# Performance work log

Measured on AMD Instinct MI355X. Metric: run time of the kernel, lower is better.

Reference implementation:

```python
import math
import jax, jax.numpy as jnp
import numpy as np

B, SEQ, N_EMBD, N_HEAD, MAX_LEN = 2, 2048, 1024, 16, 2048
D_HEAD = N_EMBD // N_HEAD


def setup_inputs() -> dict:
    key = jax.random.key(0)
    k0, k1, k2, k3, k4 = jax.random.split(key, 5)
    x = jax.random.normal(k0, (B, SEQ, N_EMBD), jnp.float32)
    # nn.Linear weights stored [out_features, in_features]; scale ~ kaiming-ish
    s = 1.0 / math.sqrt(N_EMBD)
    Wq = jax.random.normal(k1, (N_EMBD, N_EMBD), jnp.float32) * s
    Wk = jax.random.normal(k2, (N_EMBD, N_EMBD), jnp.float32) * s
    Wv = jax.random.normal(k3, (N_EMBD, N_EMBD), jnp.float32) * s
    Er = jax.random.normal(k4, (MAX_LEN, D_HEAD), jnp.float32)
    return {"x": x, "Wq": Wq, "Wk": Wk, "Wv": Wv, "Er": Er}


def _skew(QEr):
    # QEr: [B, H, S, S]; mask with anti-diagonal tril-flip, then pad/reshape skew
    S = QEr.shape[-1]
    anti = jnp.flip(jnp.tril(jnp.ones((S, S), QEr.dtype)), axis=1)
    QEr = QEr * anti  # masked_fill(mask==0, 0)
    padded = jnp.pad(QEr, ((0, 0), (0, 0), (0, 0), (1, 0)))  # [B,H,S,S+1]
    Bq, H, S_, Sp1 = padded.shape
    return padded.reshape(Bq, H, Sp1, S_)[:, :, 1:, :]  # [B,H,S,S]


def reference(x, Wq, Wk, Wv, Er):
    Bx, S, E = x.shape
    H, d = N_HEAD, D_HEAD

    def proj(W):
        return jnp.einsum('bse,fe->bsf', x, W).reshape(Bx, S, H, d).transpose(0, 2, 1, 3)

    q, k, v = proj(Wq), proj(Wk), proj(Wv)  # [B,H,S,d]
    qk = jnp.einsum('bhqd,bhkd->bhqk', q, k)
    Er_s = Er[MAX_LEN - S:, :]  # [S, d]
    QEr = jnp.einsum('bhqd,rd->bhqr', q, Er_s)  # [B,H,S,S]
    Srel = _skew(QEr)
    attn = (qk + Srel) / math.sqrt(d)
    causal = jnp.tril(jnp.ones((S, S), bool))
    attn = jnp.where(causal, attn, -jnp.inf)
    p = jax.nn.softmax(attn, axis=-1)
    out = jnp.einsum('bhqk,bhkd->bhqd', p, v)
    return out.transpose(0, 2, 1, 3).reshape(Bx, S, E)
```

## Files before the change

### kernel.cpp

```cpp
#include <hip/hip_runtime.h>
#include <hip/hip_bf16.h>
#include <stdint.h>

#define S_LEN 2048
#define EMB   1024
#define NH    16
#define DH    64
#define BATCH 2

typedef short bf16x8 __attribute__((ext_vector_type(8)));
typedef short bf16x4 __attribute__((ext_vector_type(4)));
typedef float f32x4  __attribute__((ext_vector_type(4)));

__device__ __forceinline__ unsigned short f2bf(float f) {
    union { float f; unsigned int u; } v; v.f = f;
    unsigned int r = v.u + 0x7FFFu + ((v.u >> 16) & 1u);
    return (unsigned short)(r >> 16);
}

__device__ __forceinline__ short f2bf_fast(float f) {
    __hip_bfloat16 h = __float2bfloat16(f);
    return *reinterpret_cast<short*>(&h);
}

__device__ __forceinline__ float bf2f(short s) {
    union { unsigned int u; float f; } v;
    v.u = ((unsigned int)(unsigned short)s) << 16;
    return v.f;
}

__device__ __forceinline__ bf16x8 load8f_to_bf(const float* __restrict__ p) {
    const float4* p4 = (const float4*)p;
    float4 x0 = p4[0];
    float4 x1 = p4[1];
    bf16x8 r;
    r[0] = (short)f2bf(x0.x); r[1] = (short)f2bf(x0.y);
    r[2] = (short)f2bf(x0.z); r[3] = (short)f2bf(x0.w);
    r[4] = (short)f2bf(x1.x); r[5] = (short)f2bf(x1.y);
    r[6] = (short)f2bf(x1.z); r[7] = (short)f2bf(x1.w);
    return r;
}

__device__ __forceinline__ void bar_lds() {
    asm volatile("s_waitcnt lgkmcnt(0)" ::: "memory");
    __builtin_amdgcn_sched_barrier(0);
    __builtin_amdgcn_s_barrier();
    __builtin_amdgcn_sched_barrier(0);
}

__device__ __forceinline__ void gload_lds16(const unsigned short* g, unsigned short* l) {
    __builtin_amdgcn_global_load_lds(
        (const __attribute__((address_space(1))) unsigned int*)g,
        (__attribute__((address_space(3))) unsigned int*)l, 16, 0, 0);
}

__global__ __launch_bounds__(256) void cvt_bf16(
    const float* __restrict__ x,  const float* __restrict__ wq,
    const float* __restrict__ wk, const float* __restrict__ wv,
    const float* __restrict__ er,
    unsigned short* __restrict__ xb, unsigned short* __restrict__ wb,
    unsigned short* __restrict__ erb)
{
    const int NX = 4194304 / 8, NW = 1048576 / 8, NE = 131072 / 8;
    const int total = NX + 3 * NW + NE;
    for (int i8 = blockIdx.x * 256 + threadIdx.x; i8 < total; i8 += gridDim.x * 256) {
        const float* src; unsigned short* dst; int off;
        if      (i8 < NX)          { src = x;  dst = xb;            off = i8; }
        else if (i8 < NX + NW)     { src = wq; dst = wb;            off = i8 - NX; }
        else if (i8 < NX + 2 * NW) { src = wk; dst = wb + 1048576;  off = i8 - NX - NW; }
        else if (i8 < NX + 3 * NW) { src = wv; dst = wb + 2097152;  off = i8 - NX - 2 * NW; }
        else                       { src = er; dst = erb;           off = i8 - NX - 3 * NW; }
        ((bf16x8*)dst)[off] = load8f_to_bf(src + (size_t)off * 8);
    }
}

__global__ __launch_bounds__(256) void proj_kernel_bf(
    const unsigned short* __restrict__ xb, const unsigned short* __restrict__ wb,
    unsigned short* __restrict__ Qb, unsigned short* __restrict__ Kb,
    unsigned short* __restrict__ Vt)
{
    __shared__ __align__(16) unsigned short Al[128 * 64];
    __shared__ __align__(16) unsigned short Bl[128 * 64];

    const int tid  = threadIdx.x;
    const int lane = tid & 63;
    const int w    = tid >> 6;
    const int wr   = w >> 1;
    const int wc   = w & 1;
    const int m0   = blockIdx.x * 128;
    const int c0   = blockIdx.y * 128;
    const int wsel = c0 >> 10;
    const int f0   = c0 & 1023;
    const unsigned short* __restrict__ W = wb + (size_t)wsel * 1048576;

    const int lr = lane & 15;
    const int g  = lane >> 4;

    const int srow8 = tid >> 3;
    const int scol  = (((tid & 7) ^ (srow8 & 7))) * 8;

    f32x4 acc[4][4];
#pragma unroll
    for (int i = 0; i < 4; i++)
#pragma unroll
        for (int n = 0; n < 4; n++) acc[i][n] = (f32x4){0.f, 0.f, 0.f, 0.f};

    for (int k0 = 0; k0 < 1024; k0 += 64) {
        __syncthreads();
#pragma unroll
        for (int i = 0; i < 4; i++) {
            gload_lds16(&xb[(size_t)(m0 + i * 32 + srow8) * 1024 + k0 + scol],
                        &Al[(i * 4 + w) * 512]);
            gload_lds16(&W [(size_t)(f0 + i * 32 + srow8) * 1024 + k0 + scol],
                        &Bl[(i * 4 + w) * 512]);
        }
        __syncthreads();

#pragma unroll
        for (int kk = 0; kk < 2; kk++) {
            bf16x8 a[4], b[4];
#pragma unroll
            for (int i = 0; i < 4; i++) {
                int ar = wr * 64 + i * 16 + lr;
                a[i] = *(const bf16x8*)&Al[ar * 64 + (((kk * 4 + g) ^ (ar & 7)) * 8)];
            }
#pragma unroll
            for (int n = 0; n < 4; n++) {
                int br = wc * 64 + n * 16 + lr;
                b[n] = *(const bf16x8*)&Bl[br * 64 + (((kk * 4 + g) ^ (br & 7)) * 8)];
            }
#pragma unroll
            for (int i = 0; i < 4; i++)
#pragma unroll
                for (int n = 0; n < 4; n++)
                    acc[i][n] = __builtin_amdgcn_mfma_f32_16x16x32_bf16(a[i], b[n], acc[i][n], 0, 0, 0);
        }
    }

#pragma unroll
    for (int i = 0; i < 4; i++) {
#pragma unroll
        for (int n = 0; n < 4; n++) {
#pragma unroll
            for (int j = 0; j < 4; j++) {
                int row_m = m0 + wr * 64 + i * 16 + g * 4 + j;
                int c     = c0 + wc * 64 + n * 16 + lr;
                int f     = c & 1023;
                int h     = f >> 6;
                int dd    = f & 63;
                int bb    = row_m >> 11;
                int s     = row_m & 2047;
                int bh    = bb * 16 + h;
                unsigned short bv = f2bf(acc[i][n][j]);
                if (wsel == 0)      Qb[((size_t)bh * 2048 + s) * 64 + dd] = bv;
                else if (wsel == 1) Kb[((size_t)bh * 2048 + s) * 64 + dd] = bv;
                else                Vt[((size_t)bh * 64 + dd) * 2048 + s] = bv;
            }
        }
    }
}

__global__ __launch_bounds__(256) void proj_kernel_f32(
    const float* __restrict__ x,
    const float* __restrict__ Wq, const float* __restrict__ Wk,
    const float* __restrict__ Wv,
    unsigned short* __restrict__ Qb, unsigned short* __restrict__ Kb,
    unsigned short* __restrict__ Vt)
{
    const int tid  = threadIdx.x;
    const int lane = tid & 63;
    const int w    = tid >> 6;
    const int wr   = w >> 1;
    const int wc   = w & 1;
    const int m0   = blockIdx.x * 128 + wr * 64;
    const int c0   = blockIdx.y * 128 + wc * 64;
    const int wsel = c0 >> 10;
    const int f0   = c0 & 1023;
    const float* __restrict__ W = (wsel == 0) ? Wq : (wsel == 1) ? Wk : Wv;

    const int lr = lane & 15;
    const int lk = (lane >> 4) * 8;

    f32x4 acc[4][4];
#pragma unroll
    for (int i = 0; i < 4; i++)
#pragma unroll
        for (int n = 0; n < 4; n++) acc[i][n] = (f32x4){0.f, 0.f, 0.f, 0.f};

    for (int k0 = 0; k0 < 1024; k0 += 32) {
        bf16x8 a[4], b[4];
#pragma unroll
        for (int i = 0; i < 4; i++)
            a[i] = load8f_to_bf(&x[(size_t)(m0 + i * 16 + lr) * 1024 + k0 + lk]);
#pragma unroll
        for (int n = 0; n < 4; n++)
            b[n] = load8f_to_bf(&W[(size_t)(f0 + n * 16 + lr) * 1024 + k0 + lk]);
#pragma unroll
        for (int i = 0; i < 4; i++)
#pragma unroll
            for (int n = 0; n < 4; n++)
                acc[i][n] = __builtin_amdgcn_mfma_f32_16x16x32_bf16(a[i], b[n], acc[i][n], 0, 0, 0);
    }

    const int g = lane >> 4;
#pragma unroll
    for (int i = 0; i < 4; i++) {
#pragma unroll
        for (int n = 0; n < 4; n++) {
#pragma unroll
            for (int j = 0; j < 4; j++) {
                int row_m = m0 + i * 16 + g * 4 + j;
                int c     = c0 + n * 16 + lr;
                int f     = c & 1023;
                int h     = f >> 6;
                int dd    = f & 63;
                int bb    = row_m >> 11;
                int s     = row_m & 2047;
                int bh    = bb * 16 + h;
                unsigned short bv = f2bf(acc[i][n][j]);
                if (wsel == 0)      Qb[((size_t)bh * 2048 + s) * 64 + dd] = bv;
                else if (wsel == 1) Kb[((size_t)bh * 2048 + s) * 64 + dd] = bv;
                else                Vt[((size_t)bh * 64 + dd) * 2048 + s] = bv;
            }
        }
    }
}

__global__ void cvt_er(const float* __restrict__ Er, unsigned short* __restrict__ Erb, int n)
{
    int i = blockIdx.x * 256 + threadIdx.x;
    if (i < n) Erb[i] = f2bf(Er[i]);
}

__global__ __launch_bounds__(256) void attn_kernel(
    const unsigned short* __restrict__ Qb, const unsigned short* __restrict__ Kb,
    const unsigned short* __restrict__ Vt, const unsigned short* __restrict__ Erb,
    float* __restrict__ out)
{
    __shared__ __align__(16) unsigned short Kl[64 * 64];
    __shared__ __align__(16) unsigned short Vl[64 * 64];
    __shared__ __align__(16) unsigned short El[128 * 64];
    __shared__ __align__(16) float          Rt[4][16][80];

    const int tid  = threadIdx.x;
    const int lane = tid & 63;
    const int w    = tid >> 6;

    const int i0  = blockIdx.x;
    const int xcd = i0 & 7;
    const int b2  = (i0 >> 3) & 3;
    const int qt  = 31 - (i0 >> 5);
    const int bh  = (xcd << 2) | b2;

    const int lr = lane & 15;
    const int g  = lane >> 4;
    const int lk = g * 8;

    const unsigned short* __restrict__ Qrow = Qb + (size_t)bh * 2048 * 64;
    const unsigned short* __restrict__ Krow = Kb + (size_t)bh * 2048 * 64;
    const unsigned short* __restrict__ Vrow = Vt + (size_t)bh * 64 * 2048;

    const float SCL = 0.125f * 1.44269504089f;
    const int bb  = bh >> 4;
    const int h   = bh & 15;
    const int q0  = qt * 64;
    const int q0w = q0 + w * 16;
    const int eoff = 48 - 16 * w;
    const int rbT0 = 1984 - q0;

    bf16x8 aq[2];
#pragma unroll
    for (int kk = 0; kk < 2; kk++) {
        bf16x8 q = *(const bf16x8*)&Qrow[(size_t)(q0w + lr) * 64 + kk * 32 + lk];
#pragma unroll
        for (int e = 0; e < 8; e++)
            q[e] = f2bf_fast(bf2f(q[e]) * SCL);
        aq[kk] = q;
    }

    f32x4 o[4];
#pragma unroll
    for (int m = 0; m < 4; m++) o[m] = (f32x4){0.f, 0.f, 0.f, 0.f};
    float mrow = -1e30f, lsum = 0.f;

    bf16x8 sk[2], sv[2], se[4];
    const int o8u = (tid & 7) * 8;

    auto kv_load = [&](int kt) {
        const int k0 = kt * 64;
#pragma unroll
        for (int i = 0; i < 2; i++) {
            int kr = ((i * 256 + tid) >> 3);
            sk[i] = *(const bf16x8*)&Krow[(size_t)(k0 + kr) * 64 + o8u];
        }
#pragma unroll
        for (int i = 0; i < 2; i++) {
            int d = ((i * 256 + tid) >> 3);
            sv[i] = *(const bf16x8*)&Vrow[(size_t)d * 2048 + k0 + o8u];
        }
    };
    auto kv_write = [&]() {
#pragma unroll
        for (int i = 0; i < 2; i++) {
            int kr = ((i * 256 + tid) >> 3);
            *(bf16x8*)&Kl[(kr * 64 + o8u) ^ ((kr & 7) << 3)] = sk[i];
        }
#pragma unroll
        for (int i = 0; i < 2; i++) {
            int d = ((i * 256 + tid) >> 3);
            *(bf16x8*)&Vl[(d * 64 + o8u) ^ ((d & 7) << 3)] = sv[i];
        }
    };
    auto e_load4 = [&](int base) {
#pragma unroll
        for (int i = 0; i < 4; i++) {
            int r = base + ((i * 256 + tid) >> 3);
            int rr = r > 2047 ? 2047 : r;
            se[i] = *(const bf16x8*)&Erb[(size_t)rr * 64 + o8u];
        }
    };
    auto e_load2 = [&](int base) {
#pragma unroll
        for (int i = 0; i < 2; i++) {
            int r = base + ((i * 256 + tid) >> 3);
            int rr = r > 2047 ? 2047 : r;
            se[i] = *(const bf16x8*)&Erb[(size_t)rr * 64 + o8u];
        }
    };
    auto e_write4 = [&](int base) {
#pragma unroll
        for (int i = 0; i < 4; i++) {
            int r = base + ((i * 256 + tid) >> 3);
            int slot = r & 127;
            *(bf16x8*)&El[(slot * 64 + o8u) ^ ((slot & 7) << 3)] = se[i];
        }
    };
    auto e_write2 = [&](int base) {
#pragma unroll
        for (int i = 0; i < 2; i++) {
            int r = base + ((i * 256 + tid) >> 3);
            int slot = r & 127;
            *(bf16x8*)&El[(slot * 64 + o8u) ^ ((slot & 7) << 3)] = se[i];
        }
    };

    kv_load(0);
    e_load4(rbT0);

#pragma unroll 1
    for (int kt = 0; kt <= qt; ++kt) {
        const int ep = ((qt ^ kt ^ 1) & 1) << 6;

        bar_lds();
        kv_write();
        if (kt == 0) e_write4(rbT0);
        else         e_write2(rbT0 + 64 * kt + 64);
        if (kt < qt) {
            kv_load(kt + 1);
            e_load2(rbT0 + 64 * kt + 128);
        }
        bar_lds();

        f32x4 s[4], r[5];
#pragma unroll
        for (int n = 0; n < 4; n++) s[n] = (f32x4){0.f, 0.f, 0.f, 0.f};
#pragma unroll
        for (int n = 0; n < 5; n++) r[n] = (f32x4){0.f, 0.f, 0.f, 0.f};
        __builtin_amdgcn_s_setprio(1);
#pragma unroll
        for (int kk = 0; kk < 2; kk++) {
            bf16x8 kb[4], be[5];
#pragma unroll
            for (int n = 0; n < 4; n++) {
                int kr = n * 16 + lr;
                kb[n] = *(const bf16x8*)&Kl[(kr * 64 + kk * 32 + lk) ^ ((kr & 7) << 3)];
            }
#pragma unroll
            for (int n = 0; n < 5; n++) {
                int er = (eoff + n * 16 + lr + ep) & 127;
                be[n] = *(const bf16x8*)&El[(er * 64 + kk * 32 + lk) ^ ((er & 7) << 3)];
            }
#pragma unroll
            for (int n = 0; n < 4; n++)
                s[n] = __builtin_amdgcn_mfma_f32_16x16x32_bf16(kb[n], aq[kk], s[n], 0, 0, 0);
#pragma unroll
            for (int n = 0; n < 5; n++)
                r[n] = __builtin_amdgcn_mfma_f32_16x16x32_bf16(be[n], aq[kk], r[n], 0, 0, 0);
        }
        __builtin_amdgcn_s_setprio(0);

#pragma unroll
        for (int n = 0; n < 5; n++)
            *(f32x4*)&Rt[w][lr][n * 16 + g * 4] = r[n];

        bar_lds();

        float pmax = -1e30f;
        if (kt != qt) {
#pragma unroll
            for (int n = 0; n < 4; n++)
#pragma unroll
                for (int j = 0; j < 4; j++) {
                    int kl = n * 16 + g * 4 + j;
                    float sc = s[n][j] + Rt[w][lr][kl + 15 - lr];
                    s[n][j] = sc;
                    pmax = fmaxf(pmax, sc);
                }
        } else {
#pragma unroll
            for (int n = 0; n < 4; n++)
#pragma unroll
                for (int j = 0; j < 4; j++) {
                    int kl = n * 16 + g * 4 + j;
                    float sc = s[n][j] + Rt[w][lr][kl + 15 - lr];
                    if (kl > w * 16 + lr) sc = -1e30f;
                    s[n][j] = sc;
                    pmax = fmaxf(pmax, sc);
                }
        }

        if (__any(pmax > mrow + 4.0f)) {
            pmax = fmaxf(pmax, __shfl_xor(pmax, 16));
            pmax = fmaxf(pmax, __shfl_xor(pmax, 32));
            float mn   = fmaxf(mrow, pmax);
            float corr = exp2f(mrow - mn);
            mrow = mn;
            lsum *= corr;
#pragma unroll
            for (int j = 0; j < 4; j++) {
                float cj = __shfl(corr, g * 4 + j);
#pragma unroll
                for (int m = 0; m < 4; m++) o[m][j] *= cj;
            }
        }

        float rs = 0.f;
        bf16x4 pa[4];
#pragma unroll
        for (int n = 0; n < 4; n++)
#pragma unroll
            for (int j = 0; j < 4; j++) {
                float pv = exp2f(s[n][j] - mrow);
                rs += pv;
                pa[n][j] = f2bf_fast(pv);
            }
        lsum += rs;

        __builtin_amdgcn_s_setprio(1);
#pragma unroll
        for (int m = 0; m < 4; m++) {
#pragma unroll
            for (int n = 0; n < 4; n++) {
                int d = 16 * m + lr;
                bf16x4 vb = *(const bf16x4*)&Vl[(d * 64 + 16 * n + 4 * g) ^ ((d & 7) << 3)];
                o[m] = __builtin_amdgcn_mfma_f32_16x16x16bf16_1k(pa[n], vb, o[m], 0, 0, 0);
            }
        }
        __builtin_amdgcn_s_setprio(0);
    }

    float ls = lsum;
    ls += __shfl_xor(ls, 16);
    ls += __shfl_xor(ls, 32);
    float linv = 1.0f / ls;
#pragma unroll
    for (int j = 0; j < 4; j++) {
        float lj = __shfl(linv, g * 4 + j);
#pragma unroll
        for (int m = 0; m < 4; m++) {
            int row = q0w + g * 4 + j;
            int col = h * 64 + 16 * m + lr;
            out[((size_t)bb * 2048 + row) * 1024 + col] = o[m][j] * lj;
        }
    }
}

extern "C" void kernel_launch(void* const* d_in, const int* in_sizes, int n_in,
                              void* d_out, int out_size, void* d_ws, size_t ws_size,
                              hipStream_t stream)
{
    const float* x  = (const float*)d_in[0];
    const float* Wq = (const float*)d_in[1];
    const float* Wk = (const float*)d_in[2];
    const float* Wv = (const float*)d_in[3];
    const float* Er = (const float*)d_in[4];
    float* out = (float*)d_out;

    char* ws = (char*)d_ws;
    const size_t MB = 1024 * 1024;
    unsigned short* Qb  = (unsigned short*)(ws);
    unsigned short* Kb  = (unsigned short*)(ws + 8  * MB);
    unsigned short* Vt  = (unsigned short*)(ws + 16 * MB);
    unsigned short* Erb = (unsigned short*)(ws + 24 * MB);
    unsigned short* xb  = (unsigned short*)(ws + 25 * MB);
    unsigned short* wb  = (unsigned short*)(ws + 33 * MB);

    if (ws_size >= (size_t)39 * MB) {
        cvt_bf16<<<dim3(1024), dim3(256), 0, stream>>>(x, Wq, Wk, Wv, Er, xb, wb, Erb);
        proj_kernel_bf<<<dim3(32, 24), dim3(256), 0, stream>>>(xb, wb, Qb, Kb, Vt);
    } else {
        cvt_er<<<dim3(512), dim3(256), 0, stream>>>(Er, Erb, 2048 * 64);
        proj_kernel_f32<<<dim3(32, 24), dim3(256), 0, stream>>>(x, Wq, Wk, Wv, Qb, Kb, Vt);
    }
    attn_kernel<<<dim3(1024), dim3(256), 0, stream>>>(Qb, Kb, Vt, Erb, out);
}
```

Baseline: 135.0 us.

## Double-buffer K/V and Er tiles in LDS, drop per-iteration barriers

Turns K and V into ping-pong LDS buffers and makes the Er staging a 192-row ring, so the next tile is written to LDS after the PV MFMAs instead of before compute. This leaves one workgroup barrier per iteration instead of three. The Rt scratch is transposed to a padded [80][18] layout and now guarded only by a wave-local lgkmcnt wait, since each wave reads only its own slice. LDS use rises, which may lower occupancy, and the ring-index arithmetic adds a little ALU work.

```diff
diff --git a/kernel.cpp b/kernel.cpp
--- a/kernel.cpp
+++ b/kernel.cpp
@@ -45,6 +45,11 @@
     asm volatile("s_waitcnt lgkmcnt(0)" ::: "memory");
     __builtin_amdgcn_sched_barrier(0);
     __builtin_amdgcn_s_barrier();
+    __builtin_amdgcn_sched_barrier(0);
+}
+
+__device__ __forceinline__ void fence_lds() {
+    asm volatile("s_waitcnt lgkmcnt(0)" ::: "memory");
     __builtin_amdgcn_sched_barrier(0);
 }
 
@@ -237,10 +242,10 @@
     const unsigned short* __restrict__ Vt, const unsigned short* __restrict__ Erb,
     float* __restrict__ out)
 {
-    __shared__ __align__(16) unsigned short Kl[64 * 64];
-    __shared__ __align__(16) unsigned short Vl[64 * 64];
-    __shared__ __align__(16) unsigned short El[128 * 64];
-    __shared__ __align__(16) float          Rt[4][16][80];
+    __shared__ __align__(16) unsigned short Kl[2][64 * 64];
+    __shared__ __align__(16) unsigned short Vl[2][64 * 64];
+    __shared__ __align__(16) unsigned short El[192 * 64];
+    __shared__ __align__(16) float          Rt[4][80][18];
 
     const int tid  = threadIdx.x;
     const int lane = tid & 63;
@@ -299,16 +304,16 @@
             sv[i] = *(const bf16x8*)&Vrow[(size_t)d * 2048 + k0 + o8u];
         }
     };
-    auto kv_write = [&]() {
+    auto kv_write = [&](int p) {
 #pragma unroll
         for (int i = 0; i < 2; i++) {
             int kr = ((i * 256 + tid) >> 3);
-            *(bf16x8*)&Kl[(kr * 64 + o8u) ^ ((kr & 7) << 3)] = sk[i];
+            *(bf16x8*)&Kl[p][(kr * 64 + o8u) ^ ((kr & 7) << 3)] = sk[i];
         }
 #pragma unroll
         for (int i = 0; i < 2; i++) {
             int d = ((i * 256 + tid) >> 3);
-            *(bf16x8*)&Vl[(d * 64 + o8u) ^ ((d & 7) << 3)] = sv[i];
+            *(bf16x8*)&Vl[p][(d * 64 + o8u) ^ ((d & 7) << 3)] = sv[i];
         }
     };
     auto e_load4 = [&](int base) {
@@ -327,39 +332,39 @@
             se[i] = *(const bf16x8*)&Erb[(size_t)rr * 64 + o8u];
         }
     };
-    auto e_write4 = [&](int base) {
+    auto e_write4 = [&](int bslot) {
 #pragma unroll
         for (int i = 0; i < 4; i++) {
-            int r = base + ((i * 256 + tid) >> 3);
-            int slot = r & 127;
+            int slot = bslot + ((i * 256 + tid) >> 3);
+            if (slot >= 192) slot -= 192;
             *(bf16x8*)&El[(slot * 64 + o8u) ^ ((slot & 7) << 3)] = se[i];
         }
     };
-    auto e_write2 = [&](int base) {
+    auto e_write2 = [&](int bslot) {
 #pragma unroll
         for (int i = 0; i < 2; i++) {
-            int r = base + ((i * 256 + tid) >> 3);
-            int slot = r & 127;
+            int slot = bslot + ((i * 256 + tid) >> 3);
+            if (slot >= 192) slot -= 192;
             *(bf16x8*)&El[(slot * 64 + o8u) ^ ((slot & 7) << 3)] = se[i];
         }
     };
 
+    int eb = rbT0 % 192;
     kv_load(0);
     e_load4(rbT0);
+    kv_write(0);
+    e_write4(eb);
 
 #pragma unroll 1
     for (int kt = 0; kt <= qt; ++kt) {
-        const int ep = ((qt ^ kt ^ 1) & 1) << 6;
-
         bar_lds();
-        kv_write();
-        if (kt == 0) e_write4(rbT0);
-        else         e_write2(rbT0 + 64 * kt + 64);
+
         if (kt < qt) {
             kv_load(kt + 1);
             e_load2(rbT0 + 64 * kt + 128);
         }
-        bar_lds();
+
+        const int p = kt & 1;
 
         f32x4 s[4], r[5];
 #pragma unroll
@@ -373,12 +378,13 @@
 #pragma unroll
             for (int n = 0; n < 4; n++) {
                 int kr = n * 16 + lr;
-                kb[n] = *(const bf16x8*)&Kl[(kr * 64 + kk * 32 + lk) ^ ((kr & 7) << 3)];
+                kb[n] = *(const bf16x8*)&Kl[p][(kr * 64 + kk * 32 + lk) ^ ((kr & 7) << 3)];
             }
 #pragma unroll
             for (int n = 0; n < 5; n++) {
-                int er = (eoff + n * 16 + lr + ep) & 127;
-                be[n] = *(const bf16x8*)&El[(er * 64 + kk * 32 + lk) ^ ((er & 7) << 3)];
+                int slot = eb + eoff + n * 16 + lr;
+                if (slot >= 192) slot -= 192;
+                be[n] = *(const bf16x8*)&El[(slot * 64 + kk * 32 + lk) ^ ((slot & 7) << 3)];
             }
 #pragma unroll
             for (int n = 0; n < 4; n++)
@@ -391,9 +397,11 @@
 
 #pragma unroll
         for (int n = 0; n < 5; n++)
-            *(f32x4*)&Rt[w][lr][n * 16 + g * 4] = r[n];
-
-        bar_lds();
+#pragma unroll
+            for (int j = 0; j < 4; j++)
+                Rt[w][n * 16 + g * 4 + j][lr] = r[n][j];
+
+        fence_lds();
 
         float pmax = -1e30f;
         if (kt != qt) {
@@ -402,7 +410,7 @@
 #pragma unroll
                 for (int j = 0; j < 4; j++) {
                     int kl = n * 16 + g * 4 + j;
-                    float sc = s[n][j] + Rt[w][lr][kl + 15 - lr];
+                    float sc = s[n][j] + Rt[w][kl + 15 - lr][lr];
                     s[n][j] = sc;
                     pmax = fmaxf(pmax, sc);
                 }
@@ -412,7 +420,7 @@
 #pragma unroll
                 for (int j = 0; j < 4; j++) {
                     int kl = n * 16 + g * 4 + j;
-                    float sc = s[n][j] + Rt[w][lr][kl + 15 - lr];
+                    float sc = s[n][j] + Rt[w][kl + 15 - lr][lr];
                     if (kl > w * 16 + lr) sc = -1e30f;
                     s[n][j] = sc;
                     pmax = fmaxf(pmax, sc);
@@ -452,11 +460,20 @@
 #pragma unroll
             for (int n = 0; n < 4; n++) {
                 int d = 16 * m + lr;
-                bf16x4 vb = *(const bf16x4*)&Vl[(d * 64 + 16 * n + 4 * g) ^ ((d & 7) << 3)];
+                bf16x4 vb = *(const bf16x4*)&Vl[p][(d * 64 + 16 * n + 4 * g) ^ ((d & 7) << 3)];
                 o[m] = __builtin_amdgcn_mfma_f32_16x16x16bf16_1k(pa[n], vb, o[m], 0, 0, 0);
             }
         }
         __builtin_amdgcn_s_setprio(0);
+
+        if (kt < qt) {
+            kv_write(p ^ 1);
+            int wslot = eb + 128;
+            if (wslot >= 192) wslot -= 192;
+            e_write2(wslot);
+        }
+        eb += 64;
+        if (eb >= 192) eb -= 192;
     }
 
     float ls = lsum;
```

New measurement: 130.8 us. 1.03x faster.
